# Performance work log

Measured on AMD Instinct MI355X. Metric: run time of the kernel, lower is better.

Reference implementation:

```python
import jax, jax.numpy as jnp
import numpy as np

N = 64000            # total nodes (64 graphs x 1000 nodes)
E = 1048576          # edges (~16 avg degree)
NB_NODES = 1000
NUM_GRAPHS = 64
F_IN, H1, H2, H3, OUT = 128, 256, 256, 128, 64


def setup_inputs() -> dict:
    key = jax.random.key(0)
    ks = jax.random.split(key, 12)
    x = jax.random.normal(ks[0], (N, F_IN), dtype=jnp.float32)
    # random edges within each graph: pick graph per edge, then local src/dst
    g = jax.random.randint(ks[1], (E,), 0, NUM_GRAPHS)
    src = g * NB_NODES + jax.random.randint(ks[2], (E,), 0, NB_NODES)
    dst = g * NB_NODES + jax.random.randint(ks[3], (E,), 0, NB_NODES)
    edge_index = jnp.stack([src, dst]).astype(jnp.int64)
    batch = (jnp.arange(N) // NB_NODES).astype(jnp.int64)  # sorted graph ids
    def glorot(k, fan_in, fan_out):
        s = jnp.sqrt(6.0 / (fan_in + fan_out))
        return jax.random.uniform(k, (fan_in, fan_out), jnp.float32, -s, s)
    return {
        "x": x, "edge_index": edge_index, "batch": batch,
        "W1": glorot(ks[4], F_IN, H1), "b1": jnp.zeros((H1,), jnp.float32),
        "W2": glorot(ks[5], H1, H2),   "b2": jnp.zeros((H2,), jnp.float32),
        "W3": glorot(ks[6], H2, H3),   "b3": jnp.zeros((H3,), jnp.float32),
        "Wfc": glorot(ks[7], H3 * NB_NODES, OUT),
        "bfc": jnp.zeros((OUT,), jnp.float32),
    }


def _gcn_norm(edge_index, n):
    # add self-loops, symmetric normalization D^-1/2 (A+I) D^-1/2
    loop = jnp.arange(n, dtype=edge_index.dtype)
    src = jnp.concatenate([edge_index[0], loop])
    dst = jnp.concatenate([edge_index[1], loop])
    deg = jax.ops.segment_sum(jnp.ones_like(src, jnp.float32), dst, num_segments=n)
    dinv = 1.0 / jnp.sqrt(deg)  # deg >= 1 thanks to self-loops
    norm = dinv[src] * dinv[dst]
    return src, dst, norm


def _gcn_layer(h, W, b, src, dst, norm, n):
    hl = h @ W                                   # [N, H]
    msg = hl[src] * norm[:, None]                # gather + scale
    agg = jax.ops.segment_sum(msg, dst, num_segments=n)  # scatter-add
    return agg + b


def reference(x, edge_index, batch, W1, b1, W2, b2, W3, b3, Wfc, bfc):
    n = x.shape[0]
    src, dst, norm = _gcn_norm(edge_index, n)
    h = jnp.tanh(_gcn_layer(x, W1, b1, src, dst, norm, n))
    h = jnp.tanh(_gcn_layer(h, W2, b2, src, dst, norm, n))
    h = jnp.tanh(_gcn_layer(h, W3, b3, src, dst, norm, n))
    # batch is sorted with equal graph sizes -> the per-graph loop/concat
    # in the original is exactly a reshape to [num_graphs, nodes*H3]
    h_concat = h.reshape(NUM_GRAPHS, NB_NODES * H3)
    return h_concat @ Wfc + bfc
```

## Files before the change

kernel.cpp:

```cpp
#include <hip/hip_runtime.h>
#include <math.h>

#define N_NODES 64000
#define N_EDGES 1048576
#define NB 1000
#define NG 64
#define NOUT 64
#define FC_SPLIT 500
#define BK_CAP 18000

typedef __attribute__((ext_vector_type(8))) short bfrag;
typedef __attribute__((ext_vector_type(4))) float f32x4;
typedef __attribute__((ext_vector_type(2))) float f32x2;

__device__ inline float bf2f(unsigned short u) {
    union { unsigned int i; float f; } x; x.i = ((unsigned int)u) << 16; return x.f;
}
__device__ inline float bflo(unsigned int u) {
    union { unsigned int i; float f; } x; x.i = u << 16; return x.f;
}
__device__ inline float bfhi(unsigned int u) {
    union { unsigned int i; float f; } x; x.i = u & 0xffff0000u; return x.f;
}
__device__ inline f32x2 upk(unsigned int u) {
    f32x2 r; r.x = bflo(u); r.y = bfhi(u); return r;
}
__device__ inline unsigned short f2bf(float f) {
    union { float f; unsigned int i; } x; x.f = f;
    return (unsigned short)((x.i + 0x7FFFu + ((x.i >> 16) & 1u)) >> 16);
}
__device__ inline int swz(int row, int g) { return g ^ (row & 7) ^ (g >> 3); }


__global__ __launch_bounds__(256) void k_bucket(const int* __restrict__ src,
                                                const int* __restrict__ dst,
                                                int* __restrict__ gcnt,
                                                unsigned int* __restrict__ bucket) {
    __shared__ int lcnt[64];
    __shared__ int lbase[64];
    __shared__ int lcur[64];
    int t = threadIdx.x;
    int e0 = blockIdx.x * 4096;
    if (t < 64) { lcnt[t] = 0; lcur[t] = 0; }
    __syncthreads();
    for (int i = t; i < 4096; i += 256) {
        int d = dst[e0 + i];
        int g = d / NB;
        atomicAdd(&lcnt[g], 1);
    }
    __syncthreads();
    if (t < 64) lbase[t] = atomicAdd(&gcnt[t], lcnt[t]);
    __syncthreads();
    for (int i = t; i < 4096; i += 256) {
        int d = dst[e0 + i];
        int s = src[e0 + i];
        int g = d / NB;
        int pos = atomicAdd(&lcur[g], 1);
        unsigned int packed = ((unsigned int)(d - g * NB) << 10) | (unsigned int)(s - g * NB);
        bucket[(size_t)g * BK_CAP + lbase[g] + pos] = packed;
    }
}

__global__ __launch_bounds__(1024) void k_build(const int* __restrict__ gcnt,
                                                const unsigned int* __restrict__ bucket,
                                                int* __restrict__ rowptr,
                                                int* __restrict__ rowend,
                                                float* __restrict__ dinv,
                                                unsigned short* __restrict__ colp) {
    __shared__ int ind[1024];
    __shared__ int tmp[1024];
    int t = threadIdx.x;
    int g = blockIdx.x;
    int cnt = gcnt[g];
    size_t base = (size_t)g * BK_CAP;
    ind[t] = 0;
    __syncthreads();
    for (int i = t; i < cnt; i += 1024) {
        unsigned int p = bucket[base + i];
        atomicAdd(&ind[p >> 10], 1);
    }
    __syncthreads();
    int deg = ind[t];
    if (t < NB) dinv[g * NB + t] = rsqrtf((float)(deg + 1));
    tmp[t] = deg;
    __syncthreads();
    for (int off = 1; off < 1024; off <<= 1) {
        int o = (t >= off) ? tmp[t - off] : 0;
        __syncthreads();
        tmp[t] += o;
        __syncthreads();
    }
    int excl = tmp[t] - deg;
    if (t < NB) {
        rowptr[g * NB + t] = (int)base + excl;
        rowend[g * NB + t] = (int)base + excl + deg;
    }
    ind[t] = excl;
    __syncthreads();
    for (int i = t; i < cnt; i += 1024) {
        unsigned int p = bucket[base + i];
        int dl = p >> 10;
        int pos = atomicAdd(&ind[dl], 1);
        colp[base + pos] = (unsigned short)(p & 1023u);
    }
}


__global__ void k_cast_scale(const float* __restrict__ in, const float* __restrict__ dinv,
                             unsigned short* __restrict__ out) {
    int i = (blockIdx.x * blockDim.x + threadIdx.x) * 4;
    float d = dinv[i >> 7];
    float4 v = *(const float4*)(in + i);
    union { unsigned short s[4]; uint2 u; } o;
    o.s[0] = f2bf(v.x * d); o.s[1] = f2bf(v.y * d);
    o.s[2] = f2bf(v.z * d); o.s[3] = f2bf(v.w * d);
    *(uint2*)(out + i) = o.u;
}

__global__ void k_wt(const float* __restrict__ W, unsigned short* __restrict__ Wt,
                     int K, int N) {
    int i = blockIdx.x * 256 + threadIdx.x;
    if (i < K * N) {
        int n = i / K, k = i % K;
        Wt[i] = f2bf(W[k * N + n]);
    }
}


template <int H, bool TANH>
__global__ void k_agg(const unsigned short* __restrict__ hs, unsigned short* __restrict__ op,
                      const int* __restrict__ rowptr, const int* __restrict__ rowend,
                      const unsigned short* __restrict__ col,
                      const float* __restrict__ dinv, const float* __restrict__ bias) {
    constexpr int VEC = H / 64;
    int lane = threadIdx.x & 63;
    int b = blockIdx.x;
    int c = b & 7;
    int j = b >> 3;
    int g = c + 8 * (j / 250);
    int chunk = j % 250;
    int v = g * NB + chunk * 4 + (threadIdx.x >> 6);
    const unsigned short* gb = hs + (size_t)g * NB * H;
    f32x2 a0, a1;
    {
        const unsigned short* r = hs + (size_t)v * H + lane * VEC;
        if (VEC == 2) {
            a0 = upk(*(const unsigned int*)r);
        } else {
            uint2 u = *(const uint2*)r;
            a0 = upk(u.x); a1 = upk(u.y);
        }
    }
    int beg = rowptr[v], end = rowend[v];
    for (int e0 = beg; e0 < end; e0 += 64) {
        int me = e0 + lane;
        int s = (me < end) ? (int)col[me] : 0;
        int cnt = min(64, end - e0);
        int i = 0;
        for (; i + 8 <= cnt; i += 8) {
            int sx[8];
#pragma unroll
            for (int q = 0; q < 8; ++q) sx[q] = __builtin_amdgcn_readlane(s, i + q);
            if (VEC == 2) {
                unsigned int u[8];
#pragma unroll
                for (int q = 0; q < 8; ++q)
                    u[q] = *(const unsigned int*)(gb + (size_t)sx[q] * H + lane * 2);
#pragma unroll
                for (int q = 0; q < 8; ++q) a0 += upk(u[q]);
            } else {
                uint2 u[8];
#pragma unroll
                for (int q = 0; q < 8; ++q)
                    u[q] = *(const uint2*)(gb + (size_t)sx[q] * H + lane * 4);
#pragma unroll
                for (int q = 0; q < 8; ++q) { a0 += upk(u[q].x); a1 += upk(u[q].y); }
            }
        }
        for (; i + 4 <= cnt; i += 4) {
            int sx[4];
#pragma unroll
            for (int q = 0; q < 4; ++q) sx[q] = __builtin_amdgcn_readlane(s, i + q);
            if (VEC == 2) {
                unsigned int u[4];
#pragma unroll
                for (int q = 0; q < 4; ++q)
                    u[q] = *(const unsigned int*)(gb + (size_t)sx[q] * H + lane * 2);
#pragma unroll
                for (int q = 0; q < 4; ++q) a0 += upk(u[q]);
            } else {
                uint2 u[4];
#pragma unroll
                for (int q = 0; q < 4; ++q)
                    u[q] = *(const uint2*)(gb + (size_t)sx[q] * H + lane * 4);
#pragma unroll
                for (int q = 0; q < 4; ++q) { a0 += upk(u[q].x); a1 += upk(u[q].y); }
            }
        }
        for (; i < cnt; ++i) {
            int ss = __builtin_amdgcn_readlane(s, i);
            if (VEC == 2) {
                a0 += upk(*(const unsigned int*)(gb + (size_t)ss * H + lane * 2));
            } else {
                uint2 u = *(const uint2*)(gb + (size_t)ss * H + lane * 4);
                a0 += upk(u.x); a1 += upk(u.y);
            }
        }
    }
    float dv = dinv[v];
    float acc[4];
    acc[0] = a0.x; acc[1] = a0.y;
    if (VEC == 4) { acc[2] = a1.x; acc[3] = a1.y; }
    if (TANH) {
#pragma unroll
        for (int q = 0; q < VEC; ++q) acc[q] = tanhf(acc[q] * dv + bias[lane * VEC + q]);
    } else {
#pragma unroll
        for (int q = 0; q < VEC; ++q) acc[q] *= dv;
    }
    unsigned short* o = op + (size_t)v * H + lane * VEC;
    if (VEC == 2) {
        union { unsigned short s[2]; unsigned int u; } pk;
        pk.s[0] = f2bf(acc[0]); pk.s[1] = f2bf(acc[1]);
        *(unsigned int*)o = pk.u;
    } else {
        union { unsigned short s[4]; uint2 u; } pk;
        pk.s[0] = f2bf(acc[0]); pk.s[1] = f2bf(acc[1]);
        pk.s[2] = f2bf(acc[2]); pk.s[3] = f2bf(acc[3]);
        *(uint2*)o = pk.u;
    }
}


__global__ __launch_bounds__(256) void k_gemm1(const unsigned short* __restrict__ A,
                                               const unsigned short* __restrict__ W1t,
                                               const float* __restrict__ b1,
                                               const float* __restrict__ dinv,
                                               unsigned short* __restrict__ C) {
    constexpr int K = 128, N = 256;
    __shared__ unsigned short at[64 * 136];
    int t = threadIdx.x;
    int w = t >> 6, l = t & 63;
    int lm = l & 15, lq = l >> 4;
    int m0 = blockIdx.x * 64;
    int n0 = w * 64;
    {
        int row = t >> 2, kc = (t & 3) * 32;
        const unsigned short* gr = A + (size_t)(m0 + row) * K + kc;
        unsigned short* lr = at + row * 136 + kc;
        uint4 v0 = *(const uint4*)(gr);
        uint4 v1 = *(const uint4*)(gr + 8);
        uint4 v2 = *(const uint4*)(gr + 16);
        uint4 v3 = *(const uint4*)(gr + 24);
        *(uint4*)(lr) = v0; *(uint4*)(lr + 8) = v1;
        *(uint4*)(lr + 16) = v2; *(uint4*)(lr + 24) = v3;
    }
    __syncthreads();
    f32x4 acc[4][4] = {};
    const unsigned short* Bb = W1t + (size_t)(n0 + lm) * K + lq * 8;
    bfrag bfb[2][4];
#pragma unroll
    for (int j = 0; j < 4; ++j) bfb[0][j] = *(const bfrag*)(Bb + (size_t)j * 16 * K);
#pragma unroll
    for (int it = 0; it < K / 32; ++it) {
        int ks = it * 32, cur = it & 1;
        if (it + 1 < K / 32) {
#pragma unroll
            for (int j = 0; j < 4; ++j)
                bfb[cur ^ 1][j] = *(const bfrag*)(Bb + (size_t)j * 16 * K + ks + 32);
        }
        bfrag af[4];
#pragma unroll
        for (int i = 0; i < 4; ++i) af[i] = *(const bfrag*)&at[(i * 16 + lm) * 136 + ks + lq * 8];
#pragma unroll
        for (int i = 0; i < 4; ++i)
#pragma unroll
            for (int j = 0; j < 4; ++j)
                acc[i][j] = __builtin_amdgcn_mfma_f32_16x16x32_bf16(af[i], bfb[cur][j], acc[i][j], 0, 0, 0);
    }
    float bj[4];
#pragma unroll
    for (int j = 0; j < 4; ++j) bj[j] = b1[n0 + j * 16 + lm];
    int row0 = lq * 4;
    float drow[4][4];
#pragma unroll
    for (int i = 0; i < 4; ++i)
#pragma unroll
        for (int r = 0; r < 4; ++r) drow[i][r] = dinv[m0 + i * 16 + row0 + r];
#pragma unroll
    for (int i = 0; i < 4; ++i)
#pragma unroll
        for (int j = 0; j < 4; ++j)
#pragma unroll
            for (int r = 0; r < 4; ++r) {
                float v = tanhf(acc[i][j][r] + bj[j]) * drow[i][r];
                C[(size_t)(m0 + i * 16 + row0 + r) * N + n0 + j * 16 + lm] = f2bf(v);
            }
}


__global__ __launch_bounds__(256) void k_gemm23(const unsigned short* __restrict__ A,
                                                const unsigned short* __restrict__ W2t,
                                                const float* __restrict__ b2,
                                                const unsigned short* __restrict__ W3t,
                                                const float* __restrict__ dinv,
                                                unsigned short* __restrict__ C) {
    constexpr int K = 256, N3 = 128;
    __shared__ unsigned short at[64 * 256];
    int t = threadIdx.x;
    int w = t >> 6, l = t & 63;
    int lm = l & 15, lq = l >> 4;
    int m0 = blockIdx.x * 64;
    int n0 = w * 64;
    int row0 = lq * 4;
    {
        int row = t >> 2, c = t & 3;
        const unsigned short* gr = A + (size_t)(m0 + row) * K + c * 64;
        unsigned short* lr = at + row * 256;
        uint4 v[8];
#pragma unroll
        for (int j = 0; j < 8; ++j) v[j] = *(const uint4*)(gr + j * 8);
#pragma unroll
        for (int j = 0; j < 8; ++j) {
            int gidx = c * 8 + j;
            *(uint4*)(lr + swz(row, gidx) * 8) = v[j];
        }
    }
    __syncthreads();
    f32x4 acc[4][4] = {};
    {
        const unsigned short* Bb = W2t + (size_t)(n0 + lm) * K + lq * 8;
        bfrag bfb[2][4];
#pragma unroll
        for (int j = 0; j < 4; ++j) bfb[0][j] = *(const bfrag*)(Bb + (size_t)j * 16 * K);
#pragma unroll
        for (int it = 0; it < K / 32; ++it) {
            int ks = it * 32, cur = it & 1;
            if (it + 1 < K / 32) {
#pragma unroll
                for (int j = 0; j < 4; ++j)
                    bfb[cur ^ 1][j] = *(const bfrag*)(Bb + (size_t)j * 16 * K + ks + 32);
            }
            bfrag af[4];
            int gidx = it * 4 + lq;
#pragma unroll
            for (int i = 0; i < 4; ++i) {
                int row = i * 16 + lm;
                af[i] = *(const bfrag*)&at[row * 256 + swz(row, gidx) * 8];
            }
#pragma unroll
            for (int i = 0; i < 4; ++i)
#pragma unroll
                for (int j = 0; j < 4; ++j)
                    acc[i][j] = __builtin_amdgcn_mfma_f32_16x16x32_bf16(af[i], bfb[cur][j], acc[i][j], 0, 0, 0);
        }
    }
    __syncthreads();
    {
        float bj[4];
#pragma unroll
        for (int j = 0; j < 4; ++j) bj[j] = b2[n0 + j * 16 + lm];
#pragma unroll
        for (int i = 0; i < 4; ++i)
#pragma unroll
            for (int j = 0; j < 4; ++j) {
                int colb = n0 + j * 16 + lm;
                int gidx = colb >> 3, off = colb & 7;
#pragma unroll
                for (int r = 0; r < 4; ++r) {
                    int row = i * 16 + row0 + r;
                    at[row * 256 + swz(row, gidx) * 8 + off] =
                        f2bf(tanhf(acc[i][j][r] + bj[j]));
                }
            }
    }
    __syncthreads();
    {
        f32x4 acc2[4][2] = {};
        int n3 = w * 32;
        const unsigned short* Bb = W3t + (size_t)(n3 + lm) * K + lq * 8;
        bfrag bfb[2][2];
#pragma unroll
        for (int j = 0; j < 2; ++j) bfb[0][j] = *(const bfrag*)(Bb + (size_t)j * 16 * K);
#pragma unroll
        for (int it = 0; it < K / 32; ++it) {
            int ks = it * 32, cur = it & 1;
            if (it + 1 < K / 32) {
#pragma unroll
                for (int j = 0; j < 2; ++j)
                    bfb[cur ^ 1][j] = *(const bfrag*)(Bb + (size_t)j * 16 * K + ks + 32);
            }
            bfrag af[4];
            int gidx = it * 4 + lq;
#pragma unroll
            for (int i = 0; i < 4; ++i) {
                int row = i * 16 + lm;
                af[i] = *(const bfrag*)&at[row * 256 + swz(row, gidx) * 8];
            }
#pragma unroll
            for (int i = 0; i < 4; ++i)
#pragma unroll
                for (int j = 0; j < 2; ++j)
                    acc2[i][j] = __builtin_amdgcn_mfma_f32_16x16x32_bf16(af[i], bfb[cur][j], acc2[i][j], 0, 0, 0);
        }
        float drow[4][4];
#pragma unroll
        for (int i = 0; i < 4; ++i)
#pragma unroll
            for (int r = 0; r < 4; ++r) drow[i][r] = dinv[m0 + i * 16 + row0 + r];
#pragma unroll
        for (int i = 0; i < 4; ++i)
#pragma unroll
            for (int j = 0; j < 2; ++j)
#pragma unroll
                for (int r = 0; r < 4; ++r)
                    C[(size_t)(m0 + i * 16 + row0 + r) * N3 + n3 + j * 16 + lm] =
                        f2bf(acc2[i][j][r] * drow[i][r]);
    }
}


__global__ void k_fc(const unsigned short* __restrict__ A, const float* __restrict__ B,
                     float* __restrict__ part) {
    __shared__ float As[16][68];
    __shared__ float Bs[16][68];
    const int KROW = NB * 128;
    int t = threadIdx.x;
    int tx = t & 15, ty = t >> 4;
    int k0b = blockIdx.x * 256;
    float acc[4][4] = {};
    for (int k0 = k0b; k0 < k0b + 256; k0 += 16) {
        int arow = t >> 2, ak = (t & 3) << 2;
        uint2 ua = *(const uint2*)(A + (size_t)arow * KROW + k0 + ak);
        As[ak + 0][arow] = bflo(ua.x);
        As[ak + 1][arow] = bfhi(ua.x);
        As[ak + 2][arow] = bflo(ua.y);
        As[ak + 3][arow] = bfhi(ua.y);
        int bk = t >> 4, bn4 = (t & 15) << 2;
        *(float4*)&Bs[bk][bn4] = *(const float4*)(B + (size_t)(k0 + bk) * NOUT + bn4);
        __syncthreads();
#pragma unroll
        for (int kk = 0; kk < 16; ++kk) {
            float4 a = *(const float4*)&As[kk][ty << 2];
            float4 b = *(const float4*)&Bs[kk][tx << 2];
            acc[0][0] += a.x * b.x; acc[0][1] += a.x * b.y; acc[0][2] += a.x * b.z; acc[0][3] += a.x * b.w;
            acc[1][0] += a.y * b.x; acc[1][1] += a.y * b.y; acc[1][2] += a.y * b.z; acc[1][3] += a.y * b.w;
            acc[2][0] += a.z * b.x; acc[2][1] += a.z * b.y; acc[2][2] += a.z * b.z; acc[2][3] += a.z * b.w;
            acc[3][0] += a.w * b.x; acc[3][1] += a.w * b.y; acc[3][2] += a.w * b.z; acc[3][3] += a.w * b.w;
        }
        __syncthreads();
    }
    float* po = part + (size_t)blockIdx.x * (NG * NOUT);
#pragma unroll
    for (int i = 0; i < 4; ++i) {
        float4 r;
        r.x = acc[i][0]; r.y = acc[i][1]; r.z = acc[i][2]; r.w = acc[i][3];
        *(float4*)&po[((ty << 2) + i) * NOUT + (tx << 2)] = r;
    }
}

__global__ void k_fc_reduce(const float* __restrict__ part, const float* __restrict__ bfc,
                            float* __restrict__ out) {
    int i = blockIdx.x * blockDim.x + threadIdx.x;
    float s = bfc[i & 63];
    for (int b = 0; b < FC_SPLIT; ++b) s += part[(size_t)b * (NG * NOUT) + i];
    out[i] = s;
}


static inline size_t align256(size_t x) { return (x + 255) & ~(size_t)255; }

extern "C" void kernel_launch(void* const* d_in, const int* in_sizes, int n_in,
                              void* d_out, int out_size, void* d_ws, size_t ws_size,
                              hipStream_t stream) {
    const float* x   = (const float*)d_in[0];
    const int*   ei  = (const int*)d_in[1];
    const int*   src = ei;
    const int*   dst = ei + N_EDGES;
    const float* W1  = (const float*)d_in[3];
    const float* b1  = (const float*)d_in[4];
    const float* W2  = (const float*)d_in[5];
    const float* b2  = (const float*)d_in[6];
    const float* W3  = (const float*)d_in[7];
    const float* b3  = (const float*)d_in[8];
    const float* Wfc = (const float*)d_in[9];
    const float* bfc = (const float*)d_in[10];
    float* out = (float*)d_out;

    char* w = (char*)d_ws;
    unsigned short* P0 = (unsigned short*)w; w += align256((size_t)N_NODES * 256 * 2);
    unsigned short* P1 = (unsigned short*)w; w += align256((size_t)N_NODES * 256 * 2);
    unsigned short* P2 = (unsigned short*)w; w += align256((size_t)N_NODES * 256 * 2);
    int* rowptr = (int*)w;      w += align256((size_t)N_NODES * 4);
    int* rowend = (int*)w;      w += align256((size_t)N_NODES * 4);
    float* dinv = (float*)w;    w += align256((size_t)N_NODES * 4);
    int* gcnt = (int*)w;        w += align256((size_t)NG * 4);
    unsigned int* bucket = (unsigned int*)w; w += align256((size_t)NG * BK_CAP * 4);
    unsigned short* colp = (unsigned short*)w; w += align256((size_t)NG * BK_CAP * 2);
    float* fcpart = (float*)w;  w += align256((size_t)FC_SPLIT * NG * NOUT * 4);
    unsigned short* W1t = (unsigned short*)w; w += align256((size_t)128 * 256 * 2);
    unsigned short* W2t = (unsigned short*)w; w += align256((size_t)256 * 256 * 2);
    unsigned short* W3t = (unsigned short*)w; w += align256((size_t)256 * 128 * 2);

    hipMemsetAsync(gcnt, 0, (size_t)NG * 4, stream);
    k_bucket<<<N_EDGES / 4096, 256, 0, stream>>>(src, dst, gcnt, bucket);
    k_build<<<NG, 1024, 0, stream>>>(gcnt, bucket, rowptr, rowend, dinv, colp);

    k_cast_scale<<<(N_NODES * 128 / 4) / 256, 256, 0, stream>>>(x, dinv, P0);
    k_wt<<<(128 * 256 + 255) / 256, 256, 0, stream>>>(W1, W1t, 128, 256);
    k_wt<<<(256 * 256 + 255) / 256, 256, 0, stream>>>(W2, W2t, 256, 256);
    k_wt<<<(256 * 128 + 255) / 256, 256, 0, stream>>>(W3, W3t, 256, 128);

    k_agg<128, false><<<N_NODES / 4, 256, 0, stream>>>(P0, P1, rowptr, rowend, colp, dinv, nullptr);
    k_gemm1<<<N_NODES / 64, 256, 0, stream>>>(P1, W1t, b1, dinv, P2);

    k_agg<256, false><<<N_NODES / 4, 256, 0, stream>>>(P2, P0, rowptr, rowend, colp, dinv, nullptr);
    k_gemm23<<<N_NODES / 64, 256, 0, stream>>>(P0, W2t, b2, W3t, dinv, P1);

    k_agg<128, true><<<N_NODES / 4, 256, 0, stream>>>(P1, P0, rowptr, rowend, colp, dinv, b3);

    k_fc<<<FC_SPLIT, 256, 0, stream>>>(P0, Wfc, fcpart);
    k_fc_reduce<<<NG * NOUT / 256, 256, 0, stream>>>(fcpart, bfc, out);
}
```

Baseline: 348.9 us.

## Stage weights in LDS for 1024-thread GEMMs, split gemm23, widen gather unroll and fc tile

The GEMM kernels now use 1024-thread blocks that hold the whole transposed weight matrix in swizzled LDS and read activation fragments straight from global memory. Before, each block staged an activation tile in LDS and streamed the weights from global. The fused layer-2/3 GEMM is split into separate k_gemm2 and k_gemm3 kernels, which adds a global round trip for the intermediate activations and an extra launch. Separately, the aggregation gather unroll goes from 8 to 16 edges to put more loads in flight, at a cost in registers. The fc kernel's K-chunk grows from 16 to 64 so it synchronises less often.

Result: no change. 353.1 us (+1.2%).

```diff
diff --git a/kernel.cpp b/kernel.cpp
--- a/kernel.cpp
+++ b/kernel.cpp
@@ -157,24 +157,24 @@
         int s = (me < end) ? (int)col[me] : 0;
         int cnt = min(64, end - e0);
         int i = 0;
-        for (; i + 8 <= cnt; i += 8) {
-            int sx[8];
-#pragma unroll
-            for (int q = 0; q < 8; ++q) sx[q] = __builtin_amdgcn_readlane(s, i + q);
+        for (; i + 16 <= cnt; i += 16) {
+            int sx[16];
+#pragma unroll
+            for (int q = 0; q < 16; ++q) sx[q] = __builtin_amdgcn_readlane(s, i + q);
             if (VEC == 2) {
-                unsigned int u[8];
-#pragma unroll
-                for (int q = 0; q < 8; ++q)
+                unsigned int u[16];
+#pragma unroll
+                for (int q = 0; q < 16; ++q)
                     u[q] = *(const unsigned int*)(gb + (size_t)sx[q] * H + lane * 2);
 #pragma unroll
-                for (int q = 0; q < 8; ++q) a0 += upk(u[q]);
+                for (int q = 0; q < 16; ++q) a0 += upk(u[q]);
             } else {
-                uint2 u[8];
-#pragma unroll
-                for (int q = 0; q < 8; ++q)
+                uint2 u[16];
+#pragma unroll
+                for (int q = 0; q < 16; ++q)
                     u[q] = *(const uint2*)(gb + (size_t)sx[q] * H + lane * 4);
 #pragma unroll
-                for (int q = 0; q < 8; ++q) { a0 += upk(u[q].x); a1 += upk(u[q].y); }
+                for (int q = 0; q < 16; ++q) { a0 += upk(u[q].x); a1 += upk(u[q].y); }
             }
         }
         for (; i + 4 <= cnt; i += 4) {
@@ -232,51 +232,45 @@
 }
 
 
-__global__ __launch_bounds__(256) void k_gemm1(const unsigned short* __restrict__ A,
-                                               const unsigned short* __restrict__ W1t,
-                                               const float* __restrict__ b1,
-                                               const float* __restrict__ dinv,
-                                               unsigned short* __restrict__ C) {
+__global__ __launch_bounds__(1024) void k_gemm1(const unsigned short* __restrict__ A,
+                                                const unsigned short* __restrict__ W1t,
+                                                const float* __restrict__ b1,
+                                                const float* __restrict__ dinv,
+                                                unsigned short* __restrict__ C) {
     constexpr int K = 128, N = 256;
-    __shared__ unsigned short at[64 * 136];
+    extern __shared__ unsigned short wl[];
     int t = threadIdx.x;
+    {
+        int row = t >> 2, c = t & 3;
+        const unsigned short* gr = W1t + (size_t)row * K + c * 32;
+#pragma unroll
+        for (int j = 0; j < 4; ++j) {
+            uint4 v = *(const uint4*)(gr + j * 8);
+            *(uint4*)(wl + row * K + swz(row, c * 4 + j) * 8) = v;
+        }
+    }
+    __syncthreads();
     int w = t >> 6, l = t & 63;
     int lm = l & 15, lq = l >> 4;
-    int m0 = blockIdx.x * 64;
-    int n0 = w * 64;
-    {
-        int row = t >> 2, kc = (t & 3) * 32;
-        const unsigned short* gr = A + (size_t)(m0 + row) * K + kc;
-        unsigned short* lr = at + row * 136 + kc;
-        uint4 v0 = *(const uint4*)(gr);
-        uint4 v1 = *(const uint4*)(gr + 8);
-        uint4 v2 = *(const uint4*)(gr + 16);
-        uint4 v3 = *(const uint4*)(gr + 24);
-        *(uint4*)(lr) = v0; *(uint4*)(lr + 8) = v1;
-        *(uint4*)(lr + 16) = v2; *(uint4*)(lr + 24) = v3;
-    }
-    __syncthreads();
+    int m0 = blockIdx.x * 256 + (w & 3) * 64;
+    int n0 = (w >> 2) * 64;
     f32x4 acc[4][4] = {};
-    const unsigned short* Bb = W1t + (size_t)(n0 + lm) * K + lq * 8;
-    bfrag bfb[2][4];
-#pragma unroll
-    for (int j = 0; j < 4; ++j) bfb[0][j] = *(const bfrag*)(Bb + (size_t)j * 16 * K);
 #pragma unroll
     for (int it = 0; it < K / 32; ++it) {
-        int ks = it * 32, cur = it & 1;
-        if (it + 1 < K / 32) {
+        bfrag af[4], bf[4];
+#pragma unroll
+        for (int mi = 0; mi < 4; ++mi)
+            af[mi] = *(const bfrag*)(A + (size_t)(m0 + mi * 16 + lm) * K + it * 32 + lq * 8);
+#pragma unroll
+        for (int j = 0; j < 4; ++j) {
+            int row = n0 + j * 16 + lm;
+            bf[j] = *(const bfrag*)&wl[row * K + swz(row, it * 4 + lq) * 8];
+        }
+#pragma unroll
+        for (int mi = 0; mi < 4; ++mi)
 #pragma unroll
             for (int j = 0; j < 4; ++j)
-                bfb[cur ^ 1][j] = *(const bfrag*)(Bb + (size_t)j * 16 * K + ks + 32);
-        }
-        bfrag af[4];
-#pragma unroll
-        for (int i = 0; i < 4; ++i) af[i] = *(const bfrag*)&at[(i * 16 + lm) * 136 + ks + lq * 8];
-#pragma unroll
-        for (int i = 0; i < 4; ++i)
-#pragma unroll
-            for (int j = 0; j < 4; ++j)
-                acc[i][j] = __builtin_amdgcn_mfma_f32_16x16x32_bf16(af[i], bfb[cur][j], acc[i][j], 0, 0, 0);
+                acc[mi][j] = __builtin_amdgcn_mfma_f32_16x16x32_bf16(af[mi], bf[j], acc[mi][j], 0, 0, 0);
     }
     float bj[4];
 #pragma unroll
@@ -284,163 +278,161 @@
     int row0 = lq * 4;
     float drow[4][4];
 #pragma unroll
-    for (int i = 0; i < 4; ++i)
-#pragma unroll
-        for (int r = 0; r < 4; ++r) drow[i][r] = dinv[m0 + i * 16 + row0 + r];
-#pragma unroll
-    for (int i = 0; i < 4; ++i)
+    for (int mi = 0; mi < 4; ++mi)
+#pragma unroll
+        for (int r = 0; r < 4; ++r) drow[mi][r] = dinv[m0 + mi * 16 + row0 + r];
+#pragma unroll
+    for (int mi = 0; mi < 4; ++mi)
 #pragma unroll
         for (int j = 0; j < 4; ++j)
 #pragma unroll
             for (int r = 0; r < 4; ++r) {
-                float v = tanhf(acc[i][j][r] + bj[j]) * drow[i][r];
-                C[(size_t)(m0 + i * 16 + row0 + r) * N + n0 + j * 16 + lm] = f2bf(v);
+                float v = tanhf(acc[mi][j][r] + bj[j]) * drow[mi][r];
+                C[(size_t)(m0 + mi * 16 + row0 + r) * N + n0 + j * 16 + lm] = f2bf(v);
             }
 }
 
-
-__global__ __launch_bounds__(256) void k_gemm23(const unsigned short* __restrict__ A,
+__global__ __launch_bounds__(1024) void k_gemm2(const unsigned short* __restrict__ A,
                                                 const unsigned short* __restrict__ W2t,
                                                 const float* __restrict__ b2,
+                                                unsigned short* __restrict__ C) {
+    constexpr int K = 256, N = 256;
+    extern __shared__ unsigned short wl[];
+    int t = threadIdx.x;
+    {
+        int row = t >> 2, c = t & 3;
+        const unsigned short* gr = W2t + (size_t)row * K + c * 64;
+#pragma unroll
+        for (int j = 0; j < 8; ++j) {
+            uint4 v = *(const uint4*)(gr + j * 8);
+            *(uint4*)(wl + row * K + swz(row, c * 8 + j) * 8) = v;
+        }
+    }
+    __syncthreads();
+    int w = t >> 6, l = t & 63;
+    int lm = l & 15, lq = l >> 4;
+    int m0 = blockIdx.x * 256 + (w & 3) * 64;
+    int n0 = (w >> 2) * 64;
+    f32x4 acc[4][4] = {};
+#pragma unroll
+    for (int it = 0; it < K / 32; ++it) {
+        bfrag af[4], bf[4];
+#pragma unroll
+        for (int mi = 0; mi < 4; ++mi)
+            af[mi] = *(const bfrag*)(A + (size_t)(m0 + mi * 16 + lm) * K + it * 32 + lq * 8);
+#pragma unroll
+        for (int j = 0; j < 4; ++j) {
+            int row = n0 + j * 16 + lm;
+            bf[j] = *(const bfrag*)&wl[row * K + swz(row, it * 4 + lq) * 8];
+        }
+#pragma unroll
+        for (int mi = 0; mi < 4; ++mi)
+#pragma unroll
+            for (int j = 0; j < 4; ++j)
+                acc[mi][j] = __builtin_amdgcn_mfma_f32_16x16x32_bf16(af[mi], bf[j], acc[mi][j], 0, 0, 0);
+    }
+    float bj[4];
+#pragma unroll
+    for (int j = 0; j < 4; ++j) bj[j] = b2[n0 + j * 16 + lm];
+    int row0 = lq * 4;
+#pragma unroll
+    for (int mi = 0; mi < 4; ++mi)
+#pragma unroll
+        for (int j = 0; j < 4; ++j)
+#pragma unroll
+            for (int r = 0; r < 4; ++r) {
+                float v = tanhf(acc[mi][j][r] + bj[j]);
+                C[(size_t)(m0 + mi * 16 + row0 + r) * N + n0 + j * 16 + lm] = f2bf(v);
+            }
+}
+
+__global__ __launch_bounds__(1024) void k_gemm3(const unsigned short* __restrict__ A,
                                                 const unsigned short* __restrict__ W3t,
                                                 const float* __restrict__ dinv,
                                                 unsigned short* __restrict__ C) {
     constexpr int K = 256, N3 = 128;
-    __shared__ unsigned short at[64 * 256];
+    extern __shared__ unsigned short wl[];
     int t = threadIdx.x;
+    {
+        int row = t >> 3, c = t & 7;
+        const unsigned short* gr = W3t + (size_t)row * K + c * 32;
+#pragma unroll
+        for (int j = 0; j < 4; ++j) {
+            uint4 v = *(const uint4*)(gr + j * 8);
+            *(uint4*)(wl + row * K + swz(row, c * 4 + j) * 8) = v;
+        }
+    }
+    __syncthreads();
     int w = t >> 6, l = t & 63;
     int lm = l & 15, lq = l >> 4;
-    int m0 = blockIdx.x * 64;
-    int n0 = w * 64;
+    int m0 = blockIdx.x * 256 + (w & 3) * 64;
+    int n0 = (w >> 2) * 32;
+    f32x4 acc[4][2] = {};
+#pragma unroll
+    for (int it = 0; it < K / 32; ++it) {
+        bfrag af[4], bf[2];
+#pragma unroll
+        for (int mi = 0; mi < 4; ++mi)
+            af[mi] = *(const bfrag*)(A + (size_t)(m0 + mi * 16 + lm) * K + it * 32 + lq * 8);
+#pragma unroll
+        for (int j = 0; j < 2; ++j) {
+            int row = n0 + j * 16 + lm;
+            bf[j] = *(const bfrag*)&wl[row * K + swz(row, it * 4 + lq) * 8];
+        }
+#pragma unroll
+        for (int mi = 0; mi < 4; ++mi)
+#pragma unroll
+            for (int j = 0; j < 2; ++j)
+                acc[mi][j] = __builtin_amdgcn_mfma_f32_16x16x32_bf16(af[mi], bf[j], acc[mi][j], 0, 0, 0);
+    }
     int row0 = lq * 4;
-    {
-        int row = t >> 2, c = t & 3;
-        const unsigned short* gr = A + (size_t)(m0 + row) * K + c * 64;
-        unsigned short* lr = at + row * 256;
-        uint4 v[8];
-#pragma unroll
-        for (int j = 0; j < 8; ++j) v[j] = *(const uint4*)(gr + j * 8);
-#pragma unroll
-        for (int j = 0; j < 8; ++j) {
-            int gidx = c * 8 + j;
-            *(uint4*)(lr + swz(row, gidx) * 8) = v[j];
-        }
-    }
-    __syncthreads();
-    f32x4 acc[4][4] = {};
-    {
-        const unsigned short* Bb = W2t + (size_t)(n0 + lm) * K + lq * 8;
-        bfrag bfb[2][4];
-#pragma unroll
-        for (int j = 0; j < 4; ++j) bfb[0][j] = *(const bfrag*)(Bb + (size_t)j * 16 * K);
-#pragma unroll
-        for (int it = 0; it < K / 32; ++it) {
-            int ks = it * 32, cur = it & 1;
-            if (it + 1 < K / 32) {
-#pragma unroll
-                for (int j = 0; j < 4; ++j)
-                    bfb[cur ^ 1][j] = *(const bfrag*)(Bb + (size_t)j * 16 * K + ks + 32);
-            }
-            bfrag af[4];
-            int gidx = it * 4 + lq;
-#pragma unroll
-            for (int i = 0; i < 4; ++i) {
-                int row = i * 16 + lm;
-                af[i] = *(const bfrag*)&at[row * 256 + swz(row, gidx) * 8];
-            }
-#pragma unroll
-            for (int i = 0; i < 4; ++i)
-#pragma unroll
-                for (int j = 0; j < 4; ++j)
-                    acc[i][j] = __builtin_amdgcn_mfma_f32_16x16x32_bf16(af[i], bfb[cur][j], acc[i][j], 0, 0, 0);
-        }
-    }
-    __syncthreads();
-    {
-        float bj[4];
-#pragma unroll
-        for (int j = 0; j < 4; ++j) bj[j] = b2[n0 + j * 16 + lm];
-#pragma unroll
-        for (int i = 0; i < 4; ++i)
-#pragma unroll
-            for (int j = 0; j < 4; ++j) {
-                int colb = n0 + j * 16 + lm;
-                int gidx = colb >> 3, off = colb & 7;
-#pragma unroll
-                for (int r = 0; r < 4; ++r) {
-                    int row = i * 16 + row0 + r;
-                    at[row * 256 + swz(row, gidx) * 8 + off] =
-                        f2bf(tanhf(acc[i][j][r] + bj[j]));
-                }
-            }
-    }
-    __syncthreads();
-    {
-        f32x4 acc2[4][2] = {};
-        int n3 = w * 32;
-        const unsigned short* Bb = W3t + (size_t)(n3 + lm) * K + lq * 8;
-        bfrag bfb[2][2];
-#pragma unroll
-        for (int j = 0; j < 2; ++j) bfb[0][j] = *(const bfrag*)(Bb + (size_t)j * 16 * K);
-#pragma unroll
-        for (int it = 0; it < K / 32; ++it) {
-            int ks = it * 32, cur = it & 1;
-            if (it + 1 < K / 32) {
-#pragma unroll
-                for (int j = 0; j < 2; ++j)
-                    bfb[cur ^ 1][j] = *(const bfrag*)(Bb + (size_t)j * 16 * K + ks + 32);
-            }
-            bfrag af[4];
-            int gidx = it * 4 + lq;
-#pragma unroll
-            for (int i = 0; i < 4; ++i) {
-                int row = i * 16 + lm;
-                af[i] = *(const bfrag*)&at[row * 256 + swz(row, gidx) * 8];
-            }
-#pragma unroll
-            for (int i = 0; i < 4; ++i)
-#pragma unroll
-                for (int j = 0; j < 2; ++j)
-                    acc2[i][j] = __builtin_amdgcn_mfma_f32_16x16x32_bf16(af[i], bfb[cur][j], acc2[i][j], 0, 0, 0);
-        }
-        float drow[4][4];
-#pragma unroll
-        for (int i = 0; i < 4; ++i)
-#pragma unroll
-            for (int r = 0; r < 4; ++r) drow[i][r] = dinv[m0 + i * 16 + row0 + r];
-#pragma unroll
-        for (int i = 0; i < 4; ++i)
-#pragma unroll
-            for (int j = 0; j < 2; ++j)
-#pragma unroll
-                for (int r = 0; r < 4; ++r)
-                    C[(size_t)(m0 + i * 16 + row0 + r) * N3 + n3 + j * 16 + lm] =
-                        f2bf(acc2[i][j][r] * drow[i][r]);
-    }
-}
-
-
-__global__ void k_fc(const unsigned short* __restrict__ A, const float* __restrict__ B,
-                     float* __restrict__ part) {
-    __shared__ float As[16][68];
-    __shared__ float Bs[16][68];
+    float drow[4][4];
+#pragma unroll
+    for (int mi = 0; mi < 4; ++mi)
+#pragma unroll
+        for (int r = 0; r < 4; ++r) drow[mi][r] = dinv[m0 + mi * 16 + row0 + r];
+#pragma unroll
+    for (int mi = 0; mi < 4; ++mi)
+#pragma unroll
+        for (int j = 0; j < 2; ++j)
+#pragma unroll
+            for (int r = 0; r < 4; ++r)
+                C[(size_t)(m0 + mi * 16 + row0 + r) * N3 + n0 + j * 16 + lm] =
+                    f2bf(acc[mi][j][r] * drow[mi][r]);
+}
+
+
+__global__ __launch_bounds__(256) void k_fc(const unsigned short* __restrict__ A,
+                                            const float* __restrict__ B,
+                                            float* __restrict__ part) {
+    __shared__ float As[64][68];
+    __shared__ float Bs[64][68];
     const int KROW = NB * 128;
     int t = threadIdx.x;
     int tx = t & 15, ty = t >> 4;
     int k0b = blockIdx.x * 256;
     float acc[4][4] = {};
-    for (int k0 = k0b; k0 < k0b + 256; k0 += 16) {
-        int arow = t >> 2, ak = (t & 3) << 2;
-        uint2 ua = *(const uint2*)(A + (size_t)arow * KROW + k0 + ak);
-        As[ak + 0][arow] = bflo(ua.x);
-        As[ak + 1][arow] = bfhi(ua.x);
-        As[ak + 2][arow] = bflo(ua.y);
-        As[ak + 3][arow] = bfhi(ua.y);
-        int bk = t >> 4, bn4 = (t & 15) << 2;
-        *(float4*)&Bs[bk][bn4] = *(const float4*)(B + (size_t)(k0 + bk) * NOUT + bn4);
+    for (int kc = 0; kc < 256; kc += 64) {
+        {
+            int m = t & 63, kq = (t >> 6) * 16;
+            const unsigned short* ar = A + (size_t)m * KROW + k0b + kc + kq;
+            uint4 u0 = *(const uint4*)ar;
+            uint4 u1 = *(const uint4*)(ar + 8);
+            unsigned int uu[8] = {u0.x, u0.y, u0.z, u0.w, u1.x, u1.y, u1.z, u1.w};
+#pragma unroll
+            for (int i = 0; i < 8; ++i) {
+                As[kq + 2 * i + 0][m] = bflo(uu[i]);
+                As[kq + 2 * i + 1][m] = bfhi(uu[i]);
+            }
+            int k = t >> 2, nq = (t & 3) * 16;
+            const float* br = B + (size_t)(k0b + kc + k) * NOUT + nq;
+#pragma unroll
+            for (int j = 0; j < 4; ++j)
+                *(float4*)&Bs[k][nq + j * 4] = *(const float4*)(br + j * 4);
+        }
         __syncthreads();
-#pragma unroll
-        for (int kk = 0; kk < 16; ++kk) {
+#pragma unroll 4
+        for (int kk = 0; kk < 64; ++kk) {
             float4 a = *(const float4*)&As[kk][ty << 2];
             float4 b = *(const float4*)&Bs[kk][tx << 2];
             acc[0][0] += a.x * b.x; acc[0][1] += a.x * b.y; acc[0][2] += a.x * b.z; acc[0][3] += a.x * b.w;
@@ -487,6 +479,10 @@
     const float* bfc = (const float*)d_in[10];
     float* out = (float*)d_out;
 
+    hipFuncSetAttribute((const void*)k_gemm1, hipFuncAttributeMaxDynamicSharedMemorySize, 65536);
+    hipFuncSetAttribute((const void*)k_gemm2, hipFuncAttributeMaxDynamicSharedMemorySize, 131072);
+    hipFuncSetAttribute((const void*)k_gemm3, hipFuncAttributeMaxDynamicSharedMemorySize, 65536);
+
     char* w = (char*)d_ws;
     unsigned short* P0 = (unsigned short*)w; w += align256((size_t)N_NODES * 256 * 2);
     unsigned short* P1 = (unsigned short*)w; w += align256((size_t)N_NODES * 256 * 2);
@@ -512,12 +508,13 @@
     k_wt<<<(256 * 128 + 255) / 256, 256, 0, stream>>>(W3, W3t, 256, 128);
 
     k_agg<128, false><<<N_NODES / 4, 256, 0, stream>>>(P0, P1, rowptr, rowend, colp, dinv, nullptr);
-    k_gemm1<<<N_NODES / 64, 256, 0, stream>>>(P1, W1t, b1, dinv, P2);
+    k_gemm1<<<250, 1024, 65536, stream>>>(P1, W1t, b1, dinv, P2);
 
     k_agg<256, false><<<N_NODES / 4, 256, 0, stream>>>(P2, P0, rowptr, rowend, colp, dinv, nullptr);
-    k_gemm23<<<N_NODES / 64, 256, 0, stream>>>(P0, W2t, b2, W3t, dinv, P1);
-
-    k_agg<128, true><<<N_NODES / 4, 256, 0, stream>>>(P1, P0, rowptr, rowend, colp, dinv, b3);
+    k_gemm2<<<250, 1024, 131072, stream>>>(P0, W2t, b2, P1);
+
+    k_gemm3<<<250, 1024, 65536, stream>>>(P1, W3t, dinv, P2);
+    k_agg<128, true><<<N_NODES / 4, 256, 0, stream>>>(P2, P0, rowptr, rowend, colp, dinv, b3);
 
     k_fc<<<FC_SPLIT, 256, 0, stream>>>(P0, Wfc, fcpart);
     k_fc_reduce<<<NG * NOUT / 256, 256, 0, stream>>>(fcpart, bfc, out);
```
